# Performance work log

Hardware: AMD Instinct MI355X
Metric: run time of the kernel (lower is better)

Reference implementation:

```python
import jax, jax.numpy as jnp
import numpy as np

B, P, PD = 32, 196, 768          # batch, n_subdivs, subdiv feature dim
D, H, L, NC = 768, 12, 8, 1000   # n_dims, n_heads, n_blocks, n_classes
HD = D // H                      # per-head dim (64)


def _pos_emb(n_pos, d):
    # faithful to _sinusoidal_positional_embeddings: row i (timestep) parity picks sin/cos
    i = jnp.arange(n_pos, dtype=jnp.float32)[:, None]
    j = jnp.arange(d, dtype=jnp.float32)[None, :]
    sin_v = jnp.sin(i / jnp.power(10000.0, j / d))
    cos_v = jnp.cos(i / jnp.power(10000.0, (j - 1.0) / d))
    return jnp.where((jnp.arange(n_pos)[:, None] % 2) == 0, sin_v, cos_v)  # (n_pos, d)


def _layernorm(x, g, b, eps=1e-5):
    m = jnp.mean(x, axis=-1, keepdims=True)
    v = jnp.var(x, axis=-1, keepdims=True)
    return (x - m) * jax.lax.rsqrt(v + eps) * g + b


def setup_inputs() -> dict:
    key = jax.random.key(0)
    ks = iter(jax.random.split(key, 16))
    nrm = lambda shape, s=0.02: jax.random.normal(next(ks), shape, jnp.float32) * s
    return {
        "x": jax.random.normal(next(ks), (B, P, PD), jnp.float32),
        "W_emb": nrm((PD, D)), "b_emb": jnp.zeros((D,), jnp.float32),
        "v_class": jax.random.uniform(next(ks), (1, D), jnp.float32),
        "ln1_g": jnp.ones((L, D), jnp.float32), "ln1_b": jnp.zeros((L, D), jnp.float32),
        "Wq": nrm((L, H, HD, HD)), "bq": jnp.zeros((L, H, HD), jnp.float32),
        "Wk": nrm((L, H, HD, HD)), "bk": jnp.zeros((L, H, HD), jnp.float32),
        "Wv": nrm((L, H, HD, HD)), "bv": jnp.zeros((L, H, HD), jnp.float32),
        "ln2_g": jnp.ones((L, D), jnp.float32), "ln2_b": jnp.zeros((L, D), jnp.float32),
        "W1": nrm((L, D, 4 * D)), "b1": jnp.zeros((L, 4 * D), jnp.float32),
        "W2": nrm((L, 4 * D, D)), "b2": jnp.zeros((L, D), jnp.float32),
        "W_cls": nrm((D, NC)), "b_cls": jnp.zeros((NC,), jnp.float32),
    }


def reference(x, W_emb, b_emb, v_class, ln1_g, ln1_b, Wq, bq, Wk, bk, Wv, bv,
              ln2_g, ln2_b, W1, b1, W2, b2, W_cls, b_cls):
    b = x.shape[0]
    pos = _pos_emb(P, D)                                  # (P, D), same for every sample
    h = x @ W_emb + b_emb + pos                           # (B, P, D)
    cls_tok = jnp.broadcast_to(v_class[None], (b, 1, D))
    h = jnp.concatenate([cls_tok, h], axis=1)             # (B, S, D), S = P + 1
    S = P + 1
    attns = []
    for l in range(L):
        # --- MHSA: each head reads only its own hd-slice of the input ---
        xn = _layernorm(h, ln1_g[l], ln1_b[l])
        xh = xn.reshape(b, S, H, HD)
        q = jnp.einsum('bshi,hij->bshj', xh, Wq[l]) + bq[l]
        k = jnp.einsum('bshi,hij->bshj', xh, Wk[l]) + bk[l]
        v = jnp.einsum('bshi,hij->bshj', xh, Wv[l]) + bv[l]
        scores = jnp.einsum('bqhj,bkhj->bhqk', q, k) / (HD ** 0.5)
        a = jax.nn.softmax(scores, axis=-1)               # (B, H, S, S)
        attns.append(jnp.mean(a, axis=1))                 # mean over heads, (B, S, S)
        o = jnp.einsum('bhqk,bkhj->bqhj', a, v).reshape(b, S, D)
        h = o + h                                         # residual 1
        # --- MLP ---
        xn2 = _layernorm(h, ln2_g[l], ln2_b[l])
        m = jax.nn.gelu(xn2 @ W1[l] + b1[l], approximate=False)
        h = m @ W2[l] + b2[l] + h                         # residual 2
    cls = h[:, 0]
    pred = jax.nn.softmax(cls @ W_cls + b_cls, axis=-1)   # (B, NC)
    return pred, jnp.stack(attns)                         # attns: (L, B, S, S)
```

## Files before the change

### kernel.cpp

```cpp
#include <hip/hip_runtime.h>
#include <cstdint>

typedef unsigned short u16;
typedef __attribute__((ext_vector_type(8))) short bf16x8;
typedef __attribute__((ext_vector_type(4))) float f32x4;

#define DEV static __device__ __forceinline__

#define BB 32
#define PP 196
#define DD 768
#define HH 12
#define HDD 64
#define SS 197
#define NTOK 6304
#define NTOKX 6272
#define NCLS 1000
#define DD4 3072
#define KPAD 224
#define NBH 384
#define NLAY 8

DEV u16 f2bf(float f){ unsigned u=__float_as_uint(f); u += 0x7FFFu + ((u>>16)&1u); return (u16)(u>>16); }
DEV float bf2f(u16 u){ return __uint_as_float(((unsigned)u)<<16); }

DEV float gelu_f(float x){
  float z  = 0.70710678118654752f * x;
  float az = fabsf(z);
  float t  = __builtin_amdgcn_rcpf(fmaf(0.3275911f, az, 1.f));
  float poly = t*(0.254829592f + t*(-0.284496736f + t*(1.421413741f + t*(-1.453152027f + t*1.061405429f))));
  float e  = __expf(-az*az);
  float erf_abs = 1.f - poly*e;
  float erfv = copysignf(erf_abs, x);
  return 0.5f * x * (1.f + erfv);
}

typedef __attribute__((address_space(1))) void gas1;
typedef __attribute__((address_space(3))) void las3;

DEV void gld16(const void* g, void* l){
  __builtin_amdgcn_global_load_lds((gas1*)(uintptr_t)g, (las3*)(unsigned)(uintptr_t)l, 16, 0, 0);
}

struct __align__(8) u16x4 { u16 x,y,z,w; };


__global__ void pos_kernel(float* __restrict__ pos){
  int idx = blockIdx.x*256 + threadIdx.x;
  if (idx >= PP*DD) return;
  int p = idx / DD, j = idx - p*DD;
  int odd = p & 1;
  float e = ((float)j - (float)odd) * (1.0f/(float)DD);
  float arg = (float)p / powf(10000.0f, e);
  pos[idx] = odd ? cosf(arg) : sinf(arg);
}

__global__ void f32_to_bf16_kernel(const float* __restrict__ in, u16* __restrict__ out, int n4){
  int i = blockIdx.x*256 + threadIdx.x;
  if (i >= n4) return;
  float4 v = reinterpret_cast<const float4*>(in)[i];
  u16x4 o = { f2bf(v.x), f2bf(v.y), f2bf(v.z), f2bf(v.w) };
  reinterpret_cast<u16x4*>(out)[i] = o;
}

__global__ void clstok_kernel(const float* __restrict__ vcls, float* __restrict__ h){
  int b = blockIdx.x;
  for (int i = threadIdx.x; i < DD; i += 256)
    h[(size_t)b*SS*DD + i] = vcls[i];
}

__global__ void transpose_kernel(const float* __restrict__ in, u16* __restrict__ out, int R, int C){
  __shared__ float tile[32][33];
  int bx = blockIdx.x*32, by = blockIdx.y*32;
  size_t zoff = (size_t)blockIdx.z * R * C;
  const float* src = in + zoff;
  u16* dst = out + zoff;
  int tx = threadIdx.x, ty = threadIdx.y;
  #pragma unroll
  for (int q=0;q<4;q++)
    tile[ty + q*8][tx] = src[(size_t)(by + ty + q*8)*C + bx + tx];
  __syncthreads();
  #pragma unroll
  for (int q=0;q<4;q++)
    dst[(size_t)(bx + ty + q*8)*R + by + tx] = f2bf(tile[tx][ty + q*8]);
}

__global__ void ln_stats_kernel(const float* __restrict__ h, float2* __restrict__ stats){
  int t = blockIdx.x*4 + (threadIdx.x>>6);
  int lane = threadIdx.x & 63;
  const float4* src = reinterpret_cast<const float4*>(h + (size_t)t*DD);
  float s = 0.f, s2 = 0.f;
  #pragma unroll
  for (int p=0;p<3;p++){
    float4 v = src[p*64 + lane];
    s  += v.x + v.y + v.z + v.w;
    s2 += v.x*v.x + v.y*v.y + v.z*v.z + v.w*v.w;
  }
  #pragma unroll
  for (int o=32;o>0;o>>=1){ s += __shfl_xor(s,o); s2 += __shfl_xor(s2,o); }
  if (lane == 0){
    float mean = s * (1.f/(float)DD);
    float rstd = rsqrtf(s2*(1.f/(float)DD) - mean*mean + 1e-5f);
    stats[t] = make_float2(mean, rstd);
  }
}

__global__ void ln_kernel(const float* __restrict__ h, const float* __restrict__ g,
                          const float* __restrict__ b, u16* __restrict__ xn){
  int t = blockIdx.x*4 + (threadIdx.x>>6);
  int lane = threadIdx.x & 63;
  const float4* src = reinterpret_cast<const float4*>(h + (size_t)t*DD);
  float4 xv[3];
  float s = 0.f, s2 = 0.f;
  #pragma unroll
  for (int p=0;p<3;p++){
    xv[p] = src[p*64 + lane];
    s  += xv[p].x + xv[p].y + xv[p].z + xv[p].w;
    s2 += xv[p].x*xv[p].x + xv[p].y*xv[p].y + xv[p].z*xv[p].z + xv[p].w*xv[p].w;
  }
  #pragma unroll
  for (int o=32;o>0;o>>=1){ s += __shfl_xor(s,o); s2 += __shfl_xor(s2,o); }
  float mean = s * (1.f/(float)DD);
  float rstd = rsqrtf(s2*(1.f/(float)DD) - mean*mean + 1e-5f);
  #pragma unroll
  for (int p=0;p<3;p++){
    int base = p*256 + lane*4;
    u16x4 o4 = { f2bf((xv[p].x-mean)*rstd*g[base+0]+b[base+0]),
                 f2bf((xv[p].y-mean)*rstd*g[base+1]+b[base+1]),
                 f2bf((xv[p].z-mean)*rstd*g[base+2]+b[base+2]),
                 f2bf((xv[p].w-mean)*rstd*g[base+3]+b[base+3]) };
    *reinterpret_cast<u16x4*>(&xn[(size_t)t*DD + base]) = o4;
  }
}

template<int EPI>
__global__ __launch_bounds__(256) void gemm_bf16(
    const u16* __restrict__ A, const u16* __restrict__ BT, int M, int K,
    int nbm, int nbn,
    const float* __restrict__ bias, const float* __restrict__ pos,
    float* __restrict__ Hout, u16* __restrict__ Bout)
{
  __shared__ __align__(16) u16 As[2][128*32];
  __shared__ __align__(16) u16 Bs[2][128*32];
  const int tid = threadIdx.x;
  const int wave = tid>>6, lane = tid&63;

  const int nwg = nbm*nbn;
  const int wg = blockIdx.x;
  const int xcd = wg & 7, ii = wg >> 3;
  const int q8 = nwg >> 3, r8 = nwg & 7;
  const int lin = (xcd < r8 ? xcd*(q8+1) : r8*(q8+1) + (xcd-r8)*q8) + ii;
  const int bm = lin / nbn, bn = lin - bm*nbn;

  const int wr = wave>>1, wc = wave&1;

  f32x4 acc[4][4] = {};

  const int lr = lane>>2;
  const int lc = ((lane&3) ^ ((lane>>3)&3)) * 8;
  int ar0 = bm*128 + (wave*2+0)*16 + lr; if (ar0 > M-1) ar0 = M-1;
  int ar1 = bm*128 + (wave*2+1)*16 + lr; if (ar1 > M-1) ar1 = M-1;
  const u16* aS0 = A + (size_t)ar0*K + lc;
  const u16* aS1 = A + (size_t)ar1*K + lc;
  const u16* bS0 = BT + (size_t)(bn*128 + (wave*2+0)*16 + lr)*K + lc;
  const u16* bS1 = BT + (size_t)(bn*128 + (wave*2+1)*16 + lr)*K + lc;
  const int d0 = (wave*2+0)*512;
  const int d1 = (wave*2+1)*512;

  auto stage = [&](int buf, int kt){
    gld16(aS0 + kt, &As[buf][d0]);
    gld16(aS1 + kt, &As[buf][d1]);
    gld16(bS0 + kt, &Bs[buf][d0]);
    gld16(bS1 + kt, &Bs[buf][d1]);
  };
  const int rchunk = ((lane>>4) ^ (((lane&15)>>1)&3)) * 8;
  auto compute = [&](int buf){
    bf16x8 af[4], bfv[4];
    #pragma unroll
    for (int i=0;i<4;i++)
      af[i] = *reinterpret_cast<const bf16x8*>(&As[buf][(wr*64 + i*16 + (lane&15))*32 + rchunk]);
    #pragma unroll
    for (int j=0;j<4;j++)
      bfv[j] = *reinterpret_cast<const bf16x8*>(&Bs[buf][(wc*64 + j*16 + (lane&15))*32 + rchunk]);
    #pragma unroll
    for (int i=0;i<4;i++)
      #pragma unroll
      for (int j=0;j<4;j++)
        acc[i][j] = __builtin_amdgcn_mfma_f32_16x16x32_bf16(af[i], bfv[j], acc[i][j], 0, 0, 0);
  };

  const int NT = K >> 5;
  stage(0, 0);
  int cur = 0;
  for (int t = 0; t < NT; ++t){
    if (t+1 < NT){
      stage(cur^1, (t+1)*32);
      asm volatile("s_waitcnt vmcnt(4)" ::: "memory");
    } else {
      asm volatile("s_waitcnt vmcnt(0)" ::: "memory");
    }
    __builtin_amdgcn_s_barrier();
    __builtin_amdgcn_sched_barrier(0);
    compute(cur);
    __builtin_amdgcn_s_barrier();
    cur ^= 1;
  }

  const int rowb = bm*128 + wr*64 + (lane>>4)*4;
  const int colb = bn*128 + wc*64 + (lane&15);
  const int Nst = nbn * 128;
  #pragma unroll
  for (int i=0;i<4;i++){
    #pragma unroll
    for (int j=0;j<4;j++){
      int col = colb + j*16;
      #pragma unroll
      for (int r=0;r<4;r++){
        int row = rowb + i*16 + r;
        if (row >= M) continue;
        float v = acc[i][j][r];
        if (EPI == 0){
          int bb = row / PP, p = row - bb*PP;
          Hout[((size_t)(bb*SS + 1 + p))*DD + col] = v + bias[col] + pos[p*DD + col];
        } else if (EPI == 1){
          Bout[(size_t)row*Nst + col] = f2bf(gelu_f(v + bias[col]));
        } else {
          Hout[(size_t)row*DD + col] += v + bias[col];
        }
      }
    }
  }
}

__global__ __launch_bounds__(256) void qkv_kernel(
    const float* __restrict__ h, const float2* __restrict__ stats,
    const float* __restrict__ lng, const float* __restrict__ lnb,
    const u16* __restrict__ WqT, const u16* __restrict__ WkT, const u16* __restrict__ WvT,
    const float* __restrict__ bq, const float* __restrict__ bk, const float* __restrict__ bv,
    u16* __restrict__ qb, u16* __restrict__ kb, u16* __restrict__ vb)
{
  const int LDA = 72;
  __shared__ __align__(16) u16 Asm[128*72];
  __shared__ __align__(16) u16 Wsm[3][64*72];
  const int tid = threadIdx.x, wave = tid>>6, lane = tid&63;
  const int bm = blockIdx.x, hd = blockIdx.y;

  {
    int row = tid>>1;
    int col0 = (tid&1)*32;
    int gr = bm*128 + row; if (gr > NTOK-1) gr = NTOK-1;
    float2 st = stats[gr];
    const float4* src = reinterpret_cast<const float4*>(h + (size_t)gr*DD + hd*HDD + col0);
    const float* gg = lng + hd*HDD + col0;
    const float* bb = lnb + hd*HDD + col0;
    #pragma unroll
    for (int h4=0; h4<8; ++h4){
      float4 v = src[h4];
      u16x4 o = { f2bf((v.x-st.x)*st.y*gg[h4*4+0]+bb[h4*4+0]),
                  f2bf((v.y-st.x)*st.y*gg[h4*4+1]+bb[h4*4+1]),
                  f2bf((v.z-st.x)*st.y*gg[h4*4+2]+bb[h4*4+2]),
                  f2bf((v.w-st.x)*st.y*gg[h4*4+3]+bb[h4*4+3]) };
      *reinterpret_cast<u16x4*>(&Asm[row*LDA + col0 + h4*4]) = o;
    }
  }
  const u16* wsrc[3] = { WqT + hd*4096, WkT + hd*4096, WvT + hd*4096 };
  #pragma unroll
  for (int w=0; w<3; ++w)
    #pragma unroll
    for (int ps=0; ps<2; ++ps){
      int e = (ps*256 + tid)*8;
      int row = e>>6, col = e&63;
      *reinterpret_cast<int4*>(&Wsm[w][row*LDA + col]) =
          *reinterpret_cast<const int4*>(&wsrc[w][row*64 + col]);
    }
  __syncthreads();

  bf16x8 af[2][2];
  #pragma unroll
  for (int i=0;i<2;i++)
    #pragma unroll
    for (int kk=0;kk<2;kk++)
      af[i][kk] = *reinterpret_cast<const bf16x8*>(&Asm[(wave*32 + i*16 + (lane&15))*LDA + kk*32 + (lane>>4)*8]);

  f32x4 acc[3][2][4] = {};
  #pragma unroll
  for (int w=0;w<3;w++)
    #pragma unroll
    for (int kk=0;kk<2;kk++)
      #pragma unroll
      for (int j=0;j<4;j++){
        bf16x8 bfv = *reinterpret_cast<const bf16x8*>(&Wsm[w][(j*16 + (lane&15))*LDA + kk*32 + (lane>>4)*8]);
        #pragma unroll
        for (int i=0;i<2;i++)
          acc[w][i][j] = __builtin_amdgcn_mfma_f32_16x16x32_bf16(af[i][kk], bfv, acc[w][i][j], 0,0,0);
      }

  const float* bqh = bq + hd*HDD;
  const float* bkh = bk + hd*HDD;
  const float* bvh = bv + hd*HDD;
  #pragma unroll
  for (int i=0;i<2;i++)
    #pragma unroll
    for (int j=0;j<4;j++){
      int d = j*16 + (lane&15);
      #pragma unroll
      for (int r=0;r<4;r++){
        int t = bm*128 + wave*32 + i*16 + (lane>>4)*4 + r;
        if (t >= NTOK) continue;
        int b = t / SS, sx = t - b*SS;
        size_t bh = (size_t)b*HH + hd;
        qb[(bh*SS + sx)*HDD + d] = f2bf(acc[0][i][j][r] + bqh[d]);
        kb[(bh*SS + sx)*HDD + d] = f2bf(acc[1][i][j][r] + bkh[d]);
        vb[(bh*KPAD + sx)*HDD + d] = f2bf(acc[2][i][j][r] + bvh[d]);
      }
    }
}

__global__ __launch_bounds__(256) void attn_scores_softmax_kernel(
    const u16* __restrict__ qb, const u16* __restrict__ kb, u16* __restrict__ attn)
{
  const int LDA = 72;
  __shared__ __align__(16) u16 Qs[128*72];
  __shared__ __align__(16) u16 Ks[KPAD*72];
  const int tid = threadIdx.x, wave = tid>>6, lane = tid&63;
  const int bm = blockIdx.x, bh = blockIdx.y;

  #pragma unroll
  for (int ps=0; ps<4; ++ps){
    int e = (ps*256 + tid)*8;
    int row = e>>6, col = e&63;
    int qr = bm*128 + row; if (qr > SS-1) qr = SS-1;
    *reinterpret_cast<int4*>(&Qs[row*LDA + col]) =
        *reinterpret_cast<const int4*>(&qb[((size_t)bh*SS + qr)*HDD + col]);
  }
  #pragma unroll
  for (int ps=0; ps<7; ++ps){
    int e = (ps*256 + tid)*8;
    int row = e>>6, col = e&63;
    int kr = row; if (kr > SS-1) kr = SS-1;
    *reinterpret_cast<int4*>(&Ks[row*LDA + col]) =
        *reinterpret_cast<const int4*>(&kb[((size_t)bh*SS + kr)*HDD + col]);
  }
  __syncthreads();

  bf16x8 af[2][2];
  #pragma unroll
  for (int i=0;i<2;i++)
    #pragma unroll
    for (int kk=0;kk<2;kk++)
      af[i][kk] = *reinterpret_cast<const bf16x8*>(&Qs[(wave*32 + i*16 + (lane&15))*LDA + kk*32 + (lane>>4)*8]);

  f32x4 acc[2][14];
  #pragma unroll
  for (int i=0;i<2;i++)
    #pragma unroll
    for (int j=0;j<14;j++)
      acc[i][j] = f32x4{0.f,0.f,0.f,0.f};

  #pragma unroll
  for (int kk=0;kk<2;kk++)
    #pragma unroll
    for (int j=0;j<14;j++){
      bf16x8 bfv = *reinterpret_cast<const bf16x8*>(&Ks[(j*16 + (lane&15))*LDA + kk*32 + (lane>>4)*8]);
      #pragma unroll
      for (int i=0;i<2;i++)
        acc[i][j] = __builtin_amdgcn_mfma_f32_16x16x32_bf16(af[i][kk], bfv, acc[i][j], 0,0,0);
    }

  const int kcol = lane & 15;
  #pragma unroll
  for (int i=0;i<2;i++){
    #pragma unroll
    for (int r=0;r<4;r++){
      int qg = bm*128 + wave*32 + i*16 + (lane>>4)*4 + r;
      float vals[14];
      float mx = -1e30f;
      #pragma unroll
      for (int j=0;j<14;j++){
        int kg = j*16 + kcol;
        float v = (kg < SS) ? acc[i][j][r]*0.125f : -1e30f;
        vals[j] = v;
        mx = fmaxf(mx, v);
      }
      mx = fmaxf(mx, __shfl_xor(mx,1)); mx = fmaxf(mx, __shfl_xor(mx,2));
      mx = fmaxf(mx, __shfl_xor(mx,4)); mx = fmaxf(mx, __shfl_xor(mx,8));
      float s = 0.f;
      #pragma unroll
      for (int j=0;j<14;j++){
        int kg = j*16 + kcol;
        float e = (kg < SS) ? expf(vals[j]-mx) : 0.f;
        vals[j] = e; s += e;
      }
      s += __shfl_xor(s,1); s += __shfl_xor(s,2);
      s += __shfl_xor(s,4); s += __shfl_xor(s,8);
      float inv = 1.f / s;
      if (qg < SS){
        u16* dst = attn + ((size_t)bh*SS + qg)*KPAD;
        #pragma unroll
        for (int j=0;j<14;j++)
          dst[j*16 + kcol] = f2bf(vals[j]*inv);
      }
    }
  }
}

__global__ void attnmean_kernel(const u16* __restrict__ attn, float* __restrict__ outp){
  int qi = blockIdx.x, b = blockIdx.y, kk = threadIdx.x;
  if (kk >= SS) return;
  float s = 0.f;
  #pragma unroll
  for (int h=0; h<HH; ++h)
    s += bf2f(attn[(((size_t)b*HH + h)*SS + qi)*KPAD + kk]);
  outp[((size_t)b*SS + qi)*SS + kk] = s * (1.f/12.f);
}

__global__ __launch_bounds__(256) void av_kernel(
    const u16* __restrict__ attn, const u16* __restrict__ vb, float* __restrict__ h)
{
  const int LDA = 40;
  const int LDB = 40;
  __shared__ __align__(16) u16 Asm[128*40];
  __shared__ __align__(16) u16 Bsm[64*40];
  const int tid = threadIdx.x, wave = tid>>6, lane = tid&63;
  const int bm = blockIdx.x, bh = blockIdx.y;
  const int b = bh / HH, hd = bh - b*HH;
  f32x4 acc[2][4] = {};
  for (int k0 = 0; k0 < KPAD; k0 += 32){
    if (k0) __syncthreads();
    #pragma unroll
    for (int ps=0; ps<2; ++ps){
      int e = (ps*256 + tid)*8;
      int row = e>>5, col = e&31;
      int ar = bm*128 + row; if (ar > SS-1) ar = SS-1;
      *reinterpret_cast<int4*>(&Asm[row*LDA + col]) =
          *reinterpret_cast<const int4*>(&attn[((size_t)bh*SS + ar)*KPAD + k0 + col]);
    }
    {
      int kk = tid>>3;
      int d0 = (tid&7)*8;
      bf16x8 vv = *reinterpret_cast<const bf16x8*>(&vb[((size_t)bh*KPAD + k0 + kk)*HDD + d0]);
      #pragma unroll
      for (int q=0;q<8;q++) Bsm[(d0+q)*LDB + kk] = (u16)vv[q];
    }
    __syncthreads();
    bf16x8 af[2], bfv[4];
    #pragma unroll
    for (int i=0;i<2;i++) af[i] = *reinterpret_cast<const bf16x8*>(&Asm[(wave*32 + i*16 + (lane&15))*LDA + (lane>>4)*8]);
    #pragma unroll
    for (int j=0;j<4;j++) bfv[j] = *reinterpret_cast<const bf16x8*>(&Bsm[(j*16 + (lane&15))*LDB + (lane>>4)*8]);
    #pragma unroll
    for (int i=0;i<2;i++)
      #pragma unroll
      for (int j=0;j<4;j++)
        acc[i][j] = __builtin_amdgcn_mfma_f32_16x16x32_bf16(af[i], bfv[j], acc[i][j], 0,0,0);
  }
  #pragma unroll
  for (int i=0;i<2;i++)
    #pragma unroll
    for (int j=0;j<4;j++){
      int d = j*16 + (lane&15);
      #pragma unroll
      for (int r=0;r<4;r++){
        int sx = bm*128 + wave*32 + i*16 + (lane>>4)*4 + r;
        if (sx < SS)
          h[((size_t)b*SS + sx)*DD + hd*HDD + d] += acc[i][j][r];
      }
    }
}

__global__ __launch_bounds__(256) void logits_kernel(
    const float* __restrict__ h, const float* __restrict__ Wc,
    const float* __restrict__ bc, float* __restrict__ logits)
{
  __shared__ float xs[DD];
  const int b = blockIdx.x, tid = threadIdx.x;
  for (int i = tid; i < DD; i += 256) xs[i] = h[(size_t)b*SS*DD + i];
  __syncthreads();
  const int c = blockIdx.y*250 + tid;
  if (tid >= 250 || c >= NCLS) return;
  float acc = bc[c];
  const float* wcol = Wc + c;
  #pragma unroll 16
  for (int k = 0; k < DD; ++k)
    acc += xs[k] * wcol[(size_t)k*NCLS];
  logits[(size_t)b*NCLS + c] = acc;
}

__global__ __launch_bounds__(256) void pred_softmax_kernel(
    const float* __restrict__ logits, float* __restrict__ outp)
{
  __shared__ float red[256];
  const int b = blockIdx.x, tid = threadIdx.x;
  float acc[4], mx = -1e30f;
  #pragma unroll
  for (int m=0;m<4;m++){
    int c = tid + m*256;
    acc[m] = (c < NCLS) ? logits[(size_t)b*NCLS + c] : -1e30f;
    mx = fmaxf(mx, acc[m]);
  }
  red[tid] = mx; __syncthreads();
  for (int o=128;o>0;o>>=1){ if (tid<o) red[tid] = fmaxf(red[tid], red[tid+o]); __syncthreads(); }
  mx = red[0]; __syncthreads();
  float ex[4]; float s = 0.f;
  #pragma unroll
  for (int m=0;m<4;m++){
    int c = tid + m*256;
    ex[m] = (c < NCLS) ? expf(acc[m]-mx) : 0.f;
    s += ex[m];
  }
  red[tid] = s; __syncthreads();
  for (int o=128;o>0;o>>=1){ if (tid<o) red[tid] += red[tid+o]; __syncthreads(); }
  float inv = 1.f / red[0];
  #pragma unroll
  for (int m=0;m<4;m++){
    int c = tid + m*256;
    if (c < NCLS) outp[(size_t)b*NCLS + c] = ex[m]*inv;
  }
}

extern "C" void kernel_launch(void* const* d_in, const int* in_sizes, int n_in,
                              void* d_out, int out_size, void* d_ws, size_t ws_size,
                              hipStream_t stream)
{
  const float* x      = (const float*)d_in[0];
  const float* W_emb  = (const float*)d_in[1];
  const float* b_emb  = (const float*)d_in[2];
  const float* v_class= (const float*)d_in[3];
  const float* ln1_g  = (const float*)d_in[4];
  const float* ln1_b  = (const float*)d_in[5];
  const float* Wq     = (const float*)d_in[6];
  const float* bq     = (const float*)d_in[7];
  const float* Wk     = (const float*)d_in[8];
  const float* bk     = (const float*)d_in[9];
  const float* Wv     = (const float*)d_in[10];
  const float* bv     = (const float*)d_in[11];
  const float* ln2_g  = (const float*)d_in[12];
  const float* ln2_b  = (const float*)d_in[13];
  const float* W1     = (const float*)d_in[14];
  const float* b1     = (const float*)d_in[15];
  const float* W2     = (const float*)d_in[16];
  const float* b2     = (const float*)d_in[17];
  const float* W_cls  = (const float*)d_in[18];
  const float* b_cls  = (const float*)d_in[19];
  (void)in_sizes; (void)n_in; (void)out_size;
  float* outp = (float*)d_out;

  char* ws = (char*)d_ws;
  size_t off = 0;
  auto alloc = [&](size_t bytes)->char*{
    char* p = ws + off;
    off = (off + bytes + 255) & ~((size_t)255);
    return p;
  };
  float* pos    = (float*)alloc((size_t)PP*DD*4);
  float* hbuf   = (float*)alloc((size_t)NTOK*DD*4);
  u16*   xnb    = (u16*)  alloc((size_t)NTOK*DD*2);
  float2* statsb= (float2*)alloc((size_t)NTOK*8);
  u16*   WembT  = (u16*)  alloc((size_t)DD*DD*2);
  u16*   W1Tall = (u16*)  alloc((size_t)NLAY*DD*DD4*2);
  u16*   W2Tall = (u16*)  alloc((size_t)NLAY*DD*DD4*2);
  u16*   WqT    = (u16*)  alloc((size_t)NLAY*HH*HDD*HDD*2);
  u16*   WkT    = (u16*)  alloc((size_t)NLAY*HH*HDD*HDD*2);
  u16*   WvT    = (u16*)  alloc((size_t)NLAY*HH*HDD*HDD*2);
  char*  blob   = alloc((size_t)NTOK*DD4*2);
  float* logitsb= (float*)alloc((size_t)BB*NCLS*4);
  u16* qbuf = (u16*)blob;
  u16* kbuf = qbuf + (size_t)NBH*SS*HDD;
  u16* vbuf = kbuf + (size_t)NBH*SS*HDD;
  u16* scb  = vbuf + (size_t)NBH*KPAD*HDD;
  u16* mbuf = (u16*)blob;
  u16* xbf  = scb;
  if (ws_size < off) return;

  hipMemsetAsync(vbuf, 0, (size_t)NBH*KPAD*HDD*2, stream);
  pos_kernel<<<(PP*DD+255)/256, 256, 0, stream>>>(pos);
  f32_to_bf16_kernel<<<(NTOKX*DD/4+255)/256, 256, 0, stream>>>(x, xbf, NTOKX*DD/4);
  dim3 tb(32,8);
  transpose_kernel<<<dim3(DD/32, DD/32, 1), tb, 0, stream>>>(W_emb, WembT, DD, DD);
  transpose_kernel<<<dim3(2,2,NLAY*HH), tb, 0, stream>>>(Wq, WqT, HDD, HDD);
  transpose_kernel<<<dim3(2,2,NLAY*HH), tb, 0, stream>>>(Wk, WkT, HDD, HDD);
  transpose_kernel<<<dim3(2,2,NLAY*HH), tb, 0, stream>>>(Wv, WvT, HDD, HDD);
  transpose_kernel<<<dim3(DD4/32, DD/32, NLAY), tb, 0, stream>>>(W1, W1Tall, DD, DD4);
  transpose_kernel<<<dim3(DD/32, DD4/32, NLAY), tb, 0, stream>>>(W2, W2Tall, DD4, DD);

  gemm_bf16<0><<<49*6, 256, 0, stream>>>(xbf, WembT, NTOKX, DD, 49, 6, b_emb, pos, hbuf, nullptr);
  clstok_kernel<<<BB, 256, 0, stream>>>(v_class, hbuf);

  for (int l=0; l<NLAY; ++l){
    ln_stats_kernel<<<NTOK/4, 256, 0, stream>>>(hbuf, statsb);
    qkv_kernel<<<dim3(50, HH), 256, 0, stream>>>(hbuf, statsb,
        ln1_g + l*DD, ln1_b + l*DD,
        WqT + (size_t)l*HH*4096, WkT + (size_t)l*HH*4096, WvT + (size_t)l*HH*4096,
        bq + l*HH*HDD, bk + l*HH*HDD, bv + l*HH*HDD, qbuf, kbuf, vbuf);
    attn_scores_softmax_kernel<<<dim3(2, NBH), 256, 0, stream>>>(qbuf, kbuf, scb);
    attnmean_kernel<<<dim3(SS, BB), 256, 0, stream>>>(scb, outp + 32000 + (size_t)l*BB*SS*SS);
    av_kernel<<<dim3(2, NBH), 256, 0, stream>>>(scb, vbuf, hbuf);
    ln_kernel<<<NTOK/4, 256, 0, stream>>>(hbuf, ln2_g + l*DD, ln2_b + l*DD, xnb);
    gemm_bf16<1><<<50*24, 256, 0, stream>>>(xnb, W1Tall + (size_t)l*DD*DD4, NTOK, DD, 50, 24,
                                            b1 + l*DD4, nullptr, nullptr, mbuf);
    gemm_bf16<2><<<50*6, 256, 0, stream>>>(mbuf, W2Tall + (size_t)l*DD*DD4, NTOK, DD4, 50, 6,
                                           b2 + l*DD, nullptr, hbuf, nullptr);
  }
  logits_kernel<<<dim3(BB, 4), 256, 0, stream>>>(hbuf, W_cls, b_cls, logitsb);
  pred_softmax_kernel<<<BB, 256, 0, stream>>>(logitsb, outp);
}
```

Baseline: 1.852 ms.

## Shrink GEMM workgroups to single-wave 64x64 tiles without barriers

The bf16 GEMM is changed from 256-thread workgroups computing 128x128 tiles to one-wave workgroups computing 64x64 tiles. Each wave now stages its own A and B slices into LDS, so the workgroup barriers are dropped and the wait count is adjusted for eight outstanding loads. The grids are enlarged to match. This removes barrier stalls and adds more independent workgroups, at the cost of less operand reuse across waves and more global and L2 traffic per FLOP.

```diff
diff --git a/kernel.cpp b/kernel.cpp
--- a/kernel.cpp
+++ b/kernel.cpp
@@ -134,16 +134,15 @@
 }
 
 template<int EPI>
-__global__ __launch_bounds__(256) void gemm_bf16(
+__global__ __launch_bounds__(64) void gemm_bf16(
     const u16* __restrict__ A, const u16* __restrict__ BT, int M, int K,
     int nbm, int nbn,
     const float* __restrict__ bias, const float* __restrict__ pos,
     float* __restrict__ Hout, u16* __restrict__ Bout)
 {
-  __shared__ __align__(16) u16 As[2][128*32];
-  __shared__ __align__(16) u16 Bs[2][128*32];
-  const int tid = threadIdx.x;
-  const int wave = tid>>6, lane = tid&63;
+  __shared__ __align__(16) u16 As[2][64*32];
+  __shared__ __align__(16) u16 Bs[2][64*32];
+  const int lane = threadIdx.x;
 
   const int nwg = nbm*nbn;
   const int wg = blockIdx.x;
@@ -152,36 +151,35 @@
   const int lin = (xcd < r8 ? xcd*(q8+1) : r8*(q8+1) + (xcd-r8)*q8) + ii;
   const int bm = lin / nbn, bn = lin - bm*nbn;
 
-  const int wr = wave>>1, wc = wave&1;
-
   f32x4 acc[4][4] = {};
 
   const int lr = lane>>2;
   const int lc = ((lane&3) ^ ((lane>>3)&3)) * 8;
-  int ar0 = bm*128 + (wave*2+0)*16 + lr; if (ar0 > M-1) ar0 = M-1;
-  int ar1 = bm*128 + (wave*2+1)*16 + lr; if (ar1 > M-1) ar1 = M-1;
-  const u16* aS0 = A + (size_t)ar0*K + lc;
-  const u16* aS1 = A + (size_t)ar1*K + lc;
-  const u16* bS0 = BT + (size_t)(bn*128 + (wave*2+0)*16 + lr)*K + lc;
-  const u16* bS1 = BT + (size_t)(bn*128 + (wave*2+1)*16 + lr)*K + lc;
-  const int d0 = (wave*2+0)*512;
-  const int d1 = (wave*2+1)*512;
+  const u16 *aS[4], *bS[4];
+  #pragma unroll
+  for (int g=0; g<4; ++g){
+    int ar = bm*64 + g*16 + lr; if (ar > M-1) ar = M-1;
+    aS[g] = A  + (size_t)ar*K + lc;
+    bS[g] = BT + (size_t)(bn*64 + g*16 + lr)*K + lc;
+  }
 
   auto stage = [&](int buf, int kt){
-    gld16(aS0 + kt, &As[buf][d0]);
-    gld16(aS1 + kt, &As[buf][d1]);
-    gld16(bS0 + kt, &Bs[buf][d0]);
-    gld16(bS1 + kt, &Bs[buf][d1]);
+    #pragma unroll
+    for (int g=0; g<4; ++g){
+      gld16(aS[g] + kt, &As[buf][g*512]);
+      gld16(bS[g] + kt, &Bs[buf][g*512]);
+    }
   };
   const int rchunk = ((lane>>4) ^ (((lane&15)>>1)&3)) * 8;
+  const int r15 = lane&15;
   auto compute = [&](int buf){
     bf16x8 af[4], bfv[4];
     #pragma unroll
     for (int i=0;i<4;i++)
-      af[i] = *reinterpret_cast<const bf16x8*>(&As[buf][(wr*64 + i*16 + (lane&15))*32 + rchunk]);
+      af[i] = *reinterpret_cast<const bf16x8*>(&As[buf][(i*16 + r15)*32 + rchunk]);
     #pragma unroll
     for (int j=0;j<4;j++)
-      bfv[j] = *reinterpret_cast<const bf16x8*>(&Bs[buf][(wc*64 + j*16 + (lane&15))*32 + rchunk]);
+      bfv[j] = *reinterpret_cast<const bf16x8*>(&Bs[buf][(j*16 + r15)*32 + rchunk]);
     #pragma unroll
     for (int i=0;i<4;i++)
       #pragma unroll
@@ -195,20 +193,18 @@
   for (int t = 0; t < NT; ++t){
     if (t+1 < NT){
       stage(cur^1, (t+1)*32);
-      asm volatile("s_waitcnt vmcnt(4)" ::: "memory");
+      asm volatile("s_waitcnt vmcnt(8)" ::: "memory");
     } else {
       asm volatile("s_waitcnt vmcnt(0)" ::: "memory");
     }
-    __builtin_amdgcn_s_barrier();
     __builtin_amdgcn_sched_barrier(0);
     compute(cur);
-    __builtin_amdgcn_s_barrier();
     cur ^= 1;
   }
 
-  const int rowb = bm*128 + wr*64 + (lane>>4)*4;
-  const int colb = bn*128 + wc*64 + (lane&15);
-  const int Nst = nbn * 128;
+  const int rowb = bm*64 + (lane>>4)*4;
+  const int colb = bn*64 + r15;
+  const int Nst = nbn * 64;
   #pragma unroll
   for (int i=0;i<4;i++){
     #pragma unroll
@@ -583,7 +579,7 @@
   transpose_kernel<<<dim3(DD4/32, DD/32, NLAY), tb, 0, stream>>>(W1, W1Tall, DD, DD4);
   transpose_kernel<<<dim3(DD/32, DD4/32, NLAY), tb, 0, stream>>>(W2, W2Tall, DD4, DD);
 
-  gemm_bf16<0><<<49*6, 256, 0, stream>>>(xbf, WembT, NTOKX, DD, 49, 6, b_emb, pos, hbuf, nullptr);
+  gemm_bf16<0><<<98*12, 64, 0, stream>>>(xbf, WembT, NTOKX, DD, 98, 12, b_emb, pos, hbuf, nullptr);
   clstok_kernel<<<BB, 256, 0, stream>>>(v_class, hbuf);
 
   for (int l=0; l<NLAY; ++l){
@@ -596,9 +592,9 @@
     attnmean_kernel<<<dim3(SS, BB), 256, 0, stream>>>(scb, outp + 32000 + (size_t)l*BB*SS*SS);
     av_kernel<<<dim3(2, NBH), 256, 0, stream>>>(scb, vbuf, hbuf);
     ln_kernel<<<NTOK/4, 256, 0, stream>>>(hbuf, ln2_g + l*DD, ln2_b + l*DD, xnb);
-    gemm_bf16<1><<<50*24, 256, 0, stream>>>(xnb, W1Tall + (size_t)l*DD*DD4, NTOK, DD, 50, 24,
-                                            b1 + l*DD4, nullptr, nullptr, mbuf);
-    gemm_bf16<2><<<50*6, 256, 0, stream>>>(mbuf, W2Tall + (size_t)l*DD*DD4, NTOK, DD4, 50, 6,
+    gemm_bf16<1><<<99*48, 64, 0, stream>>>(xnb, W1Tall + (size_t)l*DD*DD4, NTOK, DD, 99, 48,
+                                           b1 + l*DD4, nullptr, nullptr, mbuf);
+    gemm_bf16<2><<<99*12, 64, 0, stream>>>(mbuf, W2Tall + (size_t)l*DD*DD4, NTOK, DD4, 99, 12,
                                            b2 + l*DD, nullptr, hbuf, nullptr);
   }
   logits_kernel<<<dim3(BB, 4), 256, 0, stream>>>(hbuf, W_cls, b_cls, logitsb);
```

After: 2.299 ms. 1.24x slower.
